# Performance work log

Hardware: AMD Instinct MI355X
Metric: run time of the kernel (lower is better)

## Reference

```python
import jax, jax.numpy as jnp
import numpy as np

# model dims
B, T, D, H, FF, L, V = 2, 1024, 1024, 16, 4096, 2, 32000
DH = D // H          # head dim 64
M = 32               # num attention blocks
BS = T // M          # block size 32
TOPK = 8             # quality-selected blocks per batch element
RATIO = 0.25         # low-pass ratio for spectral quality score
THETA = 10000.0      # rope base
EPS = 1e-6


def setup_inputs() -> dict:
    key = jax.random.key(0)
    ks = jax.random.split(key, 12)
    s = 0.02
    f32 = jnp.float32
    return {
        "input_ids": jax.random.randint(ks[0], (B, T), 0, V),
        "emb": jax.random.normal(ks[1], (V, D), f32) * s,
        "wq": jax.random.normal(ks[2], (L, D, D), f32) * s,
        "wk": jax.random.normal(ks[3], (L, D, D), f32) * s,
        "wv": jax.random.normal(ks[4], (L, D, D), f32) * s,
        "wo": jax.random.normal(ks[5], (L, D, D), f32) * s,
        "w1": jax.random.normal(ks[6], (L, D, FF), f32) * s,
        "w2": jax.random.normal(ks[7], (L, FF, D), f32) * s,
        "w3": jax.random.normal(ks[8], (L, D, FF), f32) * s,
        "attn_norm": jnp.ones((L, D), f32),
        "ffn_norm": jnp.ones((L, D), f32),
        "final_norm": jnp.ones((D,), f32),
        "lm_head": jax.random.normal(ks[9], (D, V), f32) * s,
    }


def _rms(x, w):
    return x * jax.lax.rsqrt(jnp.mean(x * x, axis=-1, keepdims=True) + EPS) * w


def _rope_tables():
    inv = 1.0 / (THETA ** (jnp.arange(0, DH, 2, dtype=jnp.float32) / DH))
    pos = jnp.arange(T, dtype=jnp.float32)
    freqs = pos[:, None] * inv[None, :]            # [T, DH/2]
    emb = jnp.concatenate([freqs, freqs], axis=-1)  # [T, DH]
    return jnp.cos(emb)[None, None], jnp.sin(emb)[None, None]  # [1,1,T,DH]


def _rotate_half(x):
    h = x.shape[-1] // 2
    return jnp.concatenate([-x[..., h:], x[..., :h]], axis=-1)


def _quality_score(h):
    # spectral quality rho(t): low-frequency energy ratio along the sequence axis
    Hf = jnp.fft.rfft(h, axis=1)                   # [B, T//2+1, D] complex
    nf = Hf.shape[1]
    keep = max(1, int(nf * RATIO))
    lp_mask = (jnp.arange(nf) < keep)[None, :, None]
    h_lp = jnp.fft.irfft(jnp.where(lp_mask, Hf, 0.0), n=T, axis=1)
    return jnp.sum(h_lp * h_lp, axis=-1) / (jnp.sum(h * h, axis=-1) + EPS)  # [B,T]


def _forward(input_ids, emb, wq, wk, wv, wo, w1, w2, w3,
             attn_norm, ffn_norm, final_norm, lm_head):
    x = emb[input_ids]                             # [B,T,D]

    # per-token quality (computed once, cached across layers) -> block quality
    rho = _quality_score(x)                        # [B,T]
    blk_quality = rho.reshape(B, M, BS).mean(axis=-1)  # [B,M]

    # quality routing: select top-k blocks per batch element
    _, sel_idx = jax.lax.top_k(blk_quality, TOPK)  # [B,TOPK]
    selected = jnp.zeros((B, M), dtype=bool).at[jnp.arange(B)[:, None], sel_idx].set(True)

    # block-sparse causal mask: causal AND (kv block selected OR same block as query)
    blk_id = jnp.arange(T) // BS                   # [T]
    causal = jnp.tril(jnp.ones((T, T), dtype=bool))
    same_block = blk_id[:, None] == blk_id[None, :]
    allowed_kv = selected[:, blk_id]               # [B,T]
    mask = causal[None] & (allowed_kv[:, None, :] | same_block[None])  # [B,T,T]
    bias = jnp.where(mask, 0.0, -1e9)[:, None]     # [B,1,T,T]

    cos, sin = _rope_tables()
    scale = 1.0 / np.sqrt(DH)

    for l in range(L):
        # attention
        h = _rms(x, attn_norm[l])
        q = (h @ wq[l]).reshape(B, T, H, DH).transpose(0, 2, 1, 3)
        k = (h @ wk[l]).reshape(B, T, H, DH).transpose(0, 2, 1, 3)
        v = (h @ wv[l]).reshape(B, T, H, DH).transpose(0, 2, 1, 3)
        q = q * cos + _rotate_half(q) * sin
        k = k * cos + _rotate_half(k) * sin
        scores = jnp.einsum('bhqd,bhkd->bhqk', q, k) * scale + bias
        attn = jax.nn.softmax(scores, axis=-1)
        o = jnp.einsum('bhqk,bhkd->bhqd', attn, v).transpose(0, 2, 1, 3).reshape(B, T, D)
        x = x + o @ wo[l]
        # swiglu feed-forward
        h = _rms(x, ffn_norm[l])
        x = x + (jax.nn.silu(h @ w1[l]) * (h @ w3[l])) @ w2[l]

    x = _rms(x, final_norm)
    return x @ lm_head                             # [B,T,V]


def reference(input_ids, emb, wq, wk, wv, wo, w1, w2, w3,
              attn_norm, ffn_norm, final_norm, lm_head):
    return _forward(input_ids, emb, wq, wk, wv, wo, w1, w2, w3,
                    attn_norm, ffn_norm, final_norm, lm_head)
```

## Files before the change

kernel.cpp:

```cpp
#include <hip/hip_runtime.h>
#include <hip/hip_bf16.h>

#define Bn 2
#define Tn 1024
#define Dn 1024
#define Hn 16
#define DHn 64
#define FFn 4096
#define Ln 2
#define Vn 32000
#define GM 2048

typedef unsigned short u16;
typedef __attribute__((ext_vector_type(4))) float f4;
typedef __attribute__((ext_vector_type(4))) unsigned short us4;
typedef __attribute__((ext_vector_type(8))) unsigned short us8;
typedef __attribute__((ext_vector_type(8))) short short8;
typedef __attribute__((ext_vector_type(4))) float f32x4;

__device__ __forceinline__ u16 f2b(float x) {
  union { __hip_bfloat16 h; u16 u; } v; v.h = __float2bfloat16(x); return v.u;
}
__device__ __forceinline__ float b2f(u16 u) {
  union { unsigned int i; float f; } v; v.i = ((unsigned int)u) << 16; return v.f;
}
__device__ __forceinline__ float wred64(float v) {
#pragma unroll
  for (int m = 32; m > 0; m >>= 1) v += __shfl_xor(v, m);
  return v;
}
__device__ __forceinline__ void gload_lds16(const void* g, void* l) {
  __builtin_amdgcn_global_load_lds(
      (const __attribute__((address_space(1))) unsigned int*)g,
      (__attribute__((address_space(3))) unsigned int*)l, 16, 0, 0);
}

__global__ void rope_tab_kernel(float* COS, float* SIN) {
  int t = blockIdx.x;
  int j = threadIdx.x;
  float inv = __expf(-(float)(j & 31) * (9.210340371976184f / 32.f));
  float th = (float)t * inv;
  COS[t * 64 + j] = cosf(th);
  SIN[t * 64 + j] = sinf(th);
}

__global__ __launch_bounds__(256) void embed_kernel(const int* ids, const float* emb, float* x) {
  int g = blockIdx.x;
  int id = ids[g];
  const f4* src = (const f4*)(emb + (size_t)id * Dn);
  f4* dst = (f4*)(x + (size_t)g * Dn);
  dst[threadIdx.x] = src[threadIdx.x];
}

__global__ __launch_bounds__(256) void qa_kernel(const float* x, float* Ac, float* Bc) {
  __shared__ float ct[1024], st[1024];
  int blk = blockIdx.x;
  int b = blk >> 7, f = blk & 127;
  for (int t = threadIdx.x; t < 1024; t += 256) {
    float u = (float)((f * t) & 1023) * (6.283185307179586f / 1024.f);
    ct[t] = cosf(u); st[t] = sinf(u);
  }
  __syncthreads();
  int d0 = threadIdx.x * 4;
  f4 a = {0.f,0.f,0.f,0.f}, bb = {0.f,0.f,0.f,0.f};
  const float* xb = x + (size_t)b * Tn * Dn + d0;
  for (int t = 0; t < 1024; ++t) {
    f4 xv = *(const f4*)(xb + (size_t)t * Dn);
    float c = ct[t], s = st[t];
    a += xv * c; bb += xv * s;
  }
  size_t o = ((size_t)b * 128 + f) * Dn + d0;
  *(f4*)(Ac + o) = a; *(f4*)(Bc + o) = bb;
}

__global__ __launch_bounds__(256) void qr_kernel(const float* Ac, const float* Bc,
                                                 const float* x, float* rho) {
  __shared__ float phc[128][4], phs[128][4];
  __shared__ float redN[4], redD[4];
  int blk = blockIdx.x;
  int b = blk >> 8, t0 = (blk & 255) * 4;
  int tid = threadIdx.x;
#pragma unroll
  for (int rep = 0; rep < 2; ++rep) {
    int e = rep * 256 + tid;
    int f = e >> 2, tt = e & 3;
    float u = (float)((f * (t0 + tt)) & 1023) * (6.283185307179586f / 1024.f);
    phc[f][tt] = cosf(u); phs[f][tt] = sinf(u);
  }
  int d0 = tid * 4;
  const float* Ab = Ac + (size_t)b * 128 * Dn + d0;
  const float* Bb = Bc + (size_t)b * 128 * Dn + d0;
  f4 a0 = *(const f4*)Ab;
  float sacc[4][4];
#pragma unroll
  for (int tt = 0; tt < 4; ++tt)
#pragma unroll
    for (int c = 0; c < 4; ++c) sacc[tt][c] = 0.5f * a0[c];
  __syncthreads();
  for (int f = 1; f < 128; ++f) {
    f4 a = *(const f4*)(Ab + (size_t)f * Dn);
    f4 bb = *(const f4*)(Bb + (size_t)f * Dn);
#pragma unroll
    for (int tt = 0; tt < 4; ++tt) {
      float c = phc[f][tt], s = phs[f][tt];
#pragma unroll
      for (int e = 0; e < 4; ++e) sacc[tt][e] += a[e] * c + bb[e] * s;
    }
  }
  int wave = tid >> 6, lane = tid & 63;
  for (int tt = 0; tt < 4; ++tt) {
    f4 xv = *(const f4*)(x + ((size_t)b * Tn + t0 + tt) * Dn + d0);
    float num = 0.f, den = 0.f;
#pragma unroll
    for (int e = 0; e < 4; ++e) {
      float hl = sacc[tt][e] * (2.f / 1024.f);
      num += hl * hl;
      den += xv[e] * xv[e];
    }
    float rn = wred64(num), rd = wred64(den);
    if (lane == 0) { redN[wave] = rn; redD[wave] = rd; }
    __syncthreads();
    if (tid == 0) {
      float n = redN[0] + redN[1] + redN[2] + redN[3];
      float dd = redD[0] + redD[1] + redD[2] + redD[3];
      rho[(size_t)b * Tn + t0 + tt] = n / (dd + 1e-6f);
    }
    __syncthreads();
  }
}

__global__ void topk_kernel(const float* rho, int* sel) {
  __shared__ float bq[32];
  __shared__ int chosen[32];
  int b = blockIdx.x;
  int m = threadIdx.x;
  float s = 0.f;
  for (int j = 0; j < 32; ++j) s += rho[(size_t)b * Tn + m * 32 + j];
  bq[m] = s * (1.f / 32.f); chosen[m] = 0;
  __syncthreads();
  if (m == 0) {
    for (int it = 0; it < 8; ++it) {
      float best = -3e38f; int bi = 0;
      for (int mm = 0; mm < 32; ++mm) if (bq[mm] > best) { best = bq[mm]; bi = mm; }
      chosen[bi] = 1; bq[bi] = -3e38f;
    }
  }
  __syncthreads();
  sel[b * 32 + m] = chosen[m];
}

__global__ __launch_bounds__(256) void transpose64(const float* __restrict__ src, u16* __restrict__ dst,
                                                   int K, int N, int rowmul, int rowadd) {
  __shared__ u16 tile[64][72];
  const int n0 = blockIdx.x * 64, k0 = blockIdx.y * 64;
  const int tid = threadIdx.x;
  const int r = tid >> 2;
  const int c0 = (tid & 3) * 16;
  const float* s = src + (size_t)(k0 + r) * N + n0 + c0;
#pragma unroll
  for (int q = 0; q < 4; ++q) {
    f4 v = *(const f4*)(s + q * 4);
#pragma unroll
    for (int e = 0; e < 4; ++e) tile[c0 + q * 4 + e][r] = f2b(v[e]);
  }
  __syncthreads();
  const int n = n0 + r;
  const size_t drow = (size_t)((n >> 4) * rowmul + rowadd + (n & 15));
  us8* d = (us8*)(dst + drow * K + k0 + c0);
  us8 o0, o1;
#pragma unroll
  for (int e = 0; e < 8; ++e) { o0[e] = tile[r][c0 + e]; o1[e] = tile[r][c0 + 8 + e]; }
  d[0] = o0; d[1] = o1;
}

__global__ __launch_bounds__(256) void rmsnorm_kernel(const float* x, const float* w, u16* out) {
  __shared__ float red[4];
  int g = blockIdx.x;
  int tid = threadIdx.x;
  f4 xv = ((const f4*)(x + (size_t)g * Dn))[tid];
  float ss = xv[0]*xv[0] + xv[1]*xv[1] + xv[2]*xv[2] + xv[3]*xv[3];
  ss = wred64(ss);
  if ((tid & 63) == 0) red[tid >> 6] = ss;
  __syncthreads();
  float tot = red[0] + red[1] + red[2] + red[3];
  float r = rsqrtf(tot * (1.f / 1024.f) + 1e-6f);
  f4 wv = ((const f4*)w)[tid];
  us4 o;
#pragma unroll
  for (int e = 0; e < 4; ++e) o[e] = f2b(xv[e] * r * wv[e]);
  *(us4*)(out + (size_t)g * Dn + tid * 4) = o;
}

template<int EPI>
__global__ __launch_bounds__(256) void gemm_bf16(
    const u16* __restrict__ A, const u16* __restrict__ Bt,
    float* C, const float* R, u16* U,
    float* QRo, float* KRo, float* VRo, const float* __restrict__ COS, const float* __restrict__ SIN,
    int Ni, int Ki, int cf) {
  __shared__ short8 As[1024];
  __shared__ short8 Bs[1024];
  const int tid = threadIdx.x;
  const int wave = tid >> 6, lane = tid & 63;
  const int wr = wave >> 1, wc = wave & 1;
  const int lrow = lane & 15, lkg = lane >> 4;
  const int lg = (blockIdx.x & 7) * ((int)gridDim.x >> 3) + ((int)blockIdx.x >> 3);
  int bx, by;
  if (cf) { const int nbx = Ni >> 7; bx = lg % nbx; by = lg / nbx; }
  else    { by = lg & 15; bx = lg >> 4; }
  const size_t arow0 = (size_t)by * 128;
  const size_t bcol0 = (size_t)bx * 128;
  const f32x4 zero4 = {0.f, 0.f, 0.f, 0.f};
  f32x4 acc[4][4];
#pragma unroll
  for (int i = 0; i < 4; ++i)
#pragma unroll
    for (int j = 0; j < 4; ++j) acc[i][j] = zero4;
  const int nK = Ki >> 6;
  for (int kb = 0; kb < nK; ++kb) {
    const size_t k0 = (size_t)kb << 6;
#pragma unroll
    for (int j = 0; j < 4; ++j) {
      const int p = j * 256 + tid;
      const int r = p >> 3, c = p & 7;
      const int cs = c ^ (r & 7);
      gload_lds16(A + (arow0 + r) * Ki + k0 + cs * 8, (char*)As + p * 16);
      gload_lds16(Bt + (bcol0 + r) * Ki + k0 + cs * 8, (char*)Bs + p * 16);
    }
    __syncthreads();
#pragma unroll
    for (int kk = 0; kk < 2; ++kk) {
      short8 af[4], bfr[4];
#pragma unroll
      for (int i = 0; i < 4; ++i) {
        const int ar = wr * 64 + i * 16 + lrow;
        const int akg = kk * 4 + lkg;
        af[i] = *(const short8*)((const char*)As + ar * 128 + ((akg ^ (ar & 7)) << 4));
        const int br = wc * 64 + i * 16 + lrow;
        bfr[i] = *(const short8*)((const char*)Bs + br * 128 + ((akg ^ (br & 7)) << 4));
      }
#pragma unroll
      for (int i = 0; i < 4; ++i)
#pragma unroll
        for (int j = 0; j < 4; ++j)
          acc[i][j] = __builtin_amdgcn_mfma_f32_16x16x32_bf16(af[i], bfr[j], acc[i][j], 0, 0, 0);
    }
    __syncthreads();
  }
  const int crow = (lane >> 4) * 4;
  const int ccol = lane & 15;
  if (EPI == 0) {
#pragma unroll
    for (int i = 0; i < 4; ++i)
#pragma unroll
      for (int j = 0; j < 4; ++j)
#pragma unroll
        for (int rg = 0; rg < 4; ++rg) {
          const size_t grow = arow0 + wr * 64 + i * 16 + crow + rg;
          const size_t gcol = bcol0 + wc * 64 + j * 16 + ccol;
          float v = acc[i][j][rg];
          if (R) v += R[grow * Ni + gcol];
          C[grow * Ni + gcol] = v;
        }
  } else if (EPI == 2) {
    const int sec = (int)(bcol0 >> 10);
    const int hh = (((int)bcol0 & 1023) >> 6) + wc;
    float* dstQK = (sec == 0) ? QRo : KRo;
#pragma unroll
    for (int i = 0; i < 4; ++i)
#pragma unroll
      for (int rg = 0; rg < 4; ++rg) {
        const int t = (int)arow0 + wr * 64 + i * 16 + crow + rg;
        const int bb = t >> 10, tt = t & 1023;
        const size_t obase = ((size_t)(bb * Hn + hh) * Tn + tt) * 64;
#pragma unroll
        for (int j = 0; j < 4; ++j) {
          const int jd = j * 16 + ccol;
          const float v = acc[i][j][rg];
          if (sec < 2) {
            const float p = acc[i][j ^ 2][rg];
            const float cs = COS[tt * 64 + jd], sn = SIN[tt * 64 + jd];
            dstQK[obase + jd] = v * cs + ((j < 2) ? -p : p) * sn;
          } else {
            VRo[obase + jd] = v;
          }
        }
      }
  } else if (EPI == 3) {
#pragma unroll
    for (int i = 0; i < 4; ++i)
#pragma unroll
      for (int rg = 0; rg < 4; ++rg) {
        const size_t grow = arow0 + wr * 64 + i * 16 + crow + rg;
#pragma unroll
        for (int jp = 0; jp < 2; ++jp) {
          const int j = jp * 2;
          const float a = acc[i][j][rg];
          const float g3 = acc[i][j + 1][rg];
          const float s = (a / (1.f + __expf(-a))) * g3;
          const int f = ((((int)bcol0 + wc * 64 + j * 16) >> 5) << 4) + ccol;
          U[grow * 4096 + f] = f2b(s);
        }
      }
  }
}

__global__ __launch_bounds__(256) void attn_kernel(
    const float* __restrict__ QR, const float* __restrict__ KR, const float* __restrict__ VR,
    const int* __restrict__ sel, u16* __restrict__ O) {
  __shared__ float Qs[32][64], Ks[32][64], Vs[32][64], S[32][32];
  const int blk = blockIdx.x;
  const int mq = blk & 31, h = (blk >> 5) & 15, b = blk >> 9;
  const int tid = threadIdx.x;
  const size_t bh = (size_t)(b * Hn + h) * Tn;
  {
    const f4* q4 = (const f4*)(QR + (bh + mq * 32) * 64);
    f4* s4 = (f4*)&Qs[0][0];
    s4[tid] = q4[tid]; s4[tid + 256] = q4[tid + 256];
  }
  const int row = tid >> 3, dg = tid & 7;
  const int dh0 = dg * 8;
  f4 acc0 = {0.f,0.f,0.f,0.f}, acc1 = {0.f,0.f,0.f,0.f};
  float m_i = -3e38f, l_i = 0.f;
  for (int mk = 0; mk <= mq; ++mk) {
    if (!(sel[b * 32 + mk] | (mk == mq))) continue;
    __syncthreads();
    {
      const f4* k4 = (const f4*)(KR + (bh + mk * 32) * 64);
      const f4* v4 = (const f4*)(VR + (bh + mk * 32) * 64);
      ((f4*)Ks)[tid] = k4[tid]; ((f4*)Ks)[tid + 256] = k4[tid + 256];
      ((f4*)Vs)[tid] = v4[tid]; ((f4*)Vs)[tid + 256] = v4[tid + 256];
    }
    __syncthreads();
#pragma unroll
    for (int c = 0; c < 4; ++c) {
      const int idx = tid * 4 + c;
      const int qi = idx >> 5, kj = idx & 31;
      const f4* qv = (const f4*)Qs[qi];
      const f4* kv = (const f4*)Ks[kj];
      f4 sv = {0.f,0.f,0.f,0.f};
#pragma unroll
      for (int d = 0; d < 16; ++d) sv += qv[d] * kv[d];
      float s = (sv[0] + sv[1] + sv[2] + sv[3]) * 0.125f;
      if (mk == mq && kj > qi) s = -3e38f;
      S[qi][kj] = s;
    }
    __syncthreads();
    float mx = m_i;
#pragma unroll
    for (int j2 = 0; j2 < 32; ++j2) mx = fmaxf(mx, S[row][j2]);
    const float resc = __expf(m_i - mx);
    float pv[4]; float psum = 0.f;
#pragma unroll
    for (int c = 0; c < 4; ++c) {
      pv[c] = __expf(S[row][dg * 4 + c] - mx);
      psum += pv[c];
    }
    __syncthreads();
#pragma unroll
    for (int c = 0; c < 4; ++c) S[row][dg * 4 + c] = pv[c];
    psum += __shfl_xor(psum, 1);
    psum += __shfl_xor(psum, 2);
    psum += __shfl_xor(psum, 4);
    l_i = l_i * resc + psum;
    m_i = mx;
    acc0 *= resc; acc1 *= resc;
    __syncthreads();
#pragma unroll
    for (int kj = 0; kj < 32; ++kj) {
      const float p = S[row][kj];
      const f4* vv = (const f4*)&Vs[kj][dh0];
      acc0 += vv[0] * p; acc1 += vv[1] * p;
    }
  }
  const float inv = 1.f / l_i;
  us8 o;
#pragma unroll
  for (int e = 0; e < 4; ++e) { o[e] = f2b(acc0[e] * inv); o[4 + e] = f2b(acc1[e] * inv); }
  const int t = mq * 32 + row;
  *(us8*)(O + (size_t)(b * Tn + t) * Dn + h * 64 + dh0) = o;
}

extern "C" void kernel_launch(void* const* d_in, const int* in_sizes, int n_in,
                              void* d_out, int out_size, void* d_ws, size_t ws_size,
                              hipStream_t stream) {
  const int*   ids   = (const int*)d_in[0];
  const float* emb   = (const float*)d_in[1];
  const float* wq    = (const float*)d_in[2];
  const float* wk    = (const float*)d_in[3];
  const float* wv    = (const float*)d_in[4];
  const float* wo    = (const float*)d_in[5];
  const float* w1    = (const float*)d_in[6];
  const float* w2    = (const float*)d_in[7];
  const float* w3    = (const float*)d_in[8];
  const float* anrm  = (const float*)d_in[9];
  const float* fnrm  = (const float*)d_in[10];
  const float* finrm = (const float*)d_in[11];
  const float* lmw   = (const float*)d_in[12];
  float* out = (float*)d_out;

  char* ws = (char*)d_ws;
  size_t off = 0;
  auto alloc = [&](size_t sz) { void* p = ws + off; off += (sz + 255) & ~(size_t)255; return p; };
  const size_t MB = 1024ull * 1024ull;

  float* X    = (float*)alloc((size_t)GM * Dn * 4);
  u16*   Hb   = (u16*)alloc((size_t)GM * Dn * 2);
  float* COS  = (float*)alloc((size_t)Tn * 64 * 4);
  float* SIN  = (float*)alloc((size_t)Tn * 64 * 4);
  int*   SEL  = (int*)alloc(256);
  u16*   QKVl = (u16*)alloc((size_t)3072 * 1024 * 2);
  u16*   WOl  = (u16*)alloc((size_t)1024 * 1024 * 2);
  u16*   W13l = (u16*)alloc((size_t)8192 * 1024 * 2);
  u16*   W2l  = (u16*)alloc((size_t)1024 * 4096 * 2);
  char*  SCR  = (char*)alloc(66 * MB);

  if (off > ws_size) return;

  float* Ac  = (float*)SCR;
  float* Bc  = (float*)(SCR + 1 * MB);
  float* RHO = (float*)(SCR + 2 * MB);
  float* QRb  = (float*)(SCR + 24 * MB);
  float* KRb  = (float*)(SCR + 32 * MB);
  float* VRb  = (float*)(SCR + 40 * MB);
  u16*   Ob   = (u16*)(SCR + 48 * MB);
  u16*   Ub   = (u16*)(SCR + 0 * MB);
  u16*   LMT  = (u16*)SCR;

  rope_tab_kernel<<<Tn, 64, 0, stream>>>(COS, SIN);
  embed_kernel<<<GM, 256, 0, stream>>>(ids, emb, X);
  qa_kernel<<<Bn * 128, 256, 0, stream>>>(X, Ac, Bc);
  qr_kernel<<<Bn * 256, 256, 0, stream>>>(Ac, Bc, X, RHO);
  topk_kernel<<<Bn, 32, 0, stream>>>(RHO, SEL);

  for (int l = 0; l < Ln; ++l) {
    const size_t dd = (size_t)1024 * 1024;
    const size_t df = (size_t)1024 * 4096;
    transpose64<<<dim3(16, 16), 256, 0, stream>>>(wq + l * dd, QKVl, 1024, 1024, 16, 0);
    transpose64<<<dim3(16, 16), 256, 0, stream>>>(wk + l * dd, QKVl + dd, 1024, 1024, 16, 0);
    transpose64<<<dim3(16, 16), 256, 0, stream>>>(wv + l * dd, QKVl + 2 * dd, 1024, 1024, 16, 0);
    transpose64<<<dim3(16, 16), 256, 0, stream>>>(wo + l * dd, WOl, 1024, 1024, 16, 0);
    transpose64<<<dim3(64, 16), 256, 0, stream>>>(w1 + l * df, W13l, 1024, 4096, 32, 0);
    transpose64<<<dim3(64, 16), 256, 0, stream>>>(w3 + l * df, W13l, 1024, 4096, 32, 16);
    transpose64<<<dim3(16, 64), 256, 0, stream>>>(w2 + l * df, W2l, 4096, 1024, 16, 0);

    rmsnorm_kernel<<<GM, 256, 0, stream>>>(X, anrm + l * Dn, Hb);
    gemm_bf16<2><<<384, 256, 0, stream>>>(Hb, QKVl, nullptr, nullptr, nullptr,
                                          QRb, KRb, VRb, COS, SIN, 3072, 1024, 0);
    attn_kernel<<<Bn * Hn * 32, 256, 0, stream>>>(QRb, KRb, VRb, SEL, Ob);
    gemm_bf16<0><<<128, 256, 0, stream>>>(Ob, WOl, X, X, nullptr,
                                          nullptr, nullptr, nullptr, nullptr, nullptr, 1024, 1024, 1);
    rmsnorm_kernel<<<GM, 256, 0, stream>>>(X, fnrm + l * Dn, Hb);
    gemm_bf16<3><<<1024, 256, 0, stream>>>(Hb, W13l, nullptr, nullptr, Ub,
                                           nullptr, nullptr, nullptr, nullptr, nullptr, 8192, 1024, 0);
    gemm_bf16<0><<<128, 256, 0, stream>>>(Ub, W2l, X, X, nullptr,
                                          nullptr, nullptr, nullptr, nullptr, nullptr, 1024, 4096, 1);
  }

  transpose64<<<dim3(500, 16), 256, 0, stream>>>(lmw, LMT, 1024, Vn, 16, 0);
  rmsnorm_kernel<<<GM, 256, 0, stream>>>(X, finrm, Hb);
  gemm_bf16<0><<<4000, 256, 0, stream>>>(Hb, LMT, out, nullptr, nullptr,
                                         nullptr, nullptr, nullptr, nullptr, nullptr, Vn, 1024, 0);
}
```

Baseline: 1.582 ms.

## Split spectral projection over time chunks, double-buffer GEMM LDS, nontemporal stores

The spectral-projection kernel now splits the sequence into 8 time chunks, giving 2048 blocks instead of 256. A new reduction kernel sums the chunk partials, which exposes more parallelism at the cost of extra partial-buffer traffic and one more launch. The bf16 GEMM double-buffers its LDS tiles so the next K-tile loads are issued before the current tile's MFMAs run. GEMM outputs with no residual are now written with nontemporal stores. The extra LDS doubles shared memory per block, which may lower occupancy.

```diff
diff --git a/kernel.cpp b/kernel.cpp
--- a/kernel.cpp
+++ b/kernel.cpp
@@ -52,25 +52,44 @@
   dst[threadIdx.x] = src[threadIdx.x];
 }
 
-__global__ __launch_bounds__(256) void qa_kernel(const float* x, float* Ac, float* Bc) {
-  __shared__ float ct[1024], st[1024];
+__global__ __launch_bounds__(256) void qa_kernel(const float* __restrict__ x,
+                                                 float* __restrict__ PA, float* __restrict__ PB) {
+  __shared__ float ct[128], st[128];
   int blk = blockIdx.x;
-  int b = blk >> 7, f = blk & 127;
-  for (int t = threadIdx.x; t < 1024; t += 256) {
+  int tc = blk & 7, f = (blk >> 3) & 127, b = blk >> 10;
+  int t0 = tc * 128;
+  if (threadIdx.x < 128) {
+    int t = t0 + threadIdx.x;
     float u = (float)((f * t) & 1023) * (6.283185307179586f / 1024.f);
-    ct[t] = cosf(u); st[t] = sinf(u);
+    ct[threadIdx.x] = cosf(u); st[threadIdx.x] = sinf(u);
   }
   __syncthreads();
   int d0 = threadIdx.x * 4;
   f4 a = {0.f,0.f,0.f,0.f}, bb = {0.f,0.f,0.f,0.f};
-  const float* xb = x + (size_t)b * Tn * Dn + d0;
-  for (int t = 0; t < 1024; ++t) {
+  const float* xb = x + ((size_t)b * Tn + t0) * Dn + d0;
+  for (int t = 0; t < 128; ++t) {
     f4 xv = *(const f4*)(xb + (size_t)t * Dn);
     float c = ct[t], s = st[t];
     a += xv * c; bb += xv * s;
   }
-  size_t o = ((size_t)b * 128 + f) * Dn + d0;
-  *(f4*)(Ac + o) = a; *(f4*)(Bc + o) = bb;
+  size_t o = (((size_t)b * 128 + f) * 8 + tc) * Dn + d0;
+  *(f4*)(PA + o) = a; *(f4*)(PB + o) = bb;
+}
+
+__global__ __launch_bounds__(256) void qa_red_kernel(const float* __restrict__ PA, const float* __restrict__ PB,
+                                                     float* __restrict__ Ac, float* __restrict__ Bc) {
+  int blk = blockIdx.x;
+  int d0 = threadIdx.x * 4;
+  const float* pa = PA + ((size_t)blk * 8) * Dn + d0;
+  const float* pb = PB + ((size_t)blk * 8) * Dn + d0;
+  f4 a = {0.f,0.f,0.f,0.f}, bb = {0.f,0.f,0.f,0.f};
+#pragma unroll
+  for (int tc = 0; tc < 8; ++tc) {
+    a += *(const f4*)(pa + (size_t)tc * Dn);
+    bb += *(const f4*)(pb + (size_t)tc * Dn);
+  }
+  *(f4*)(Ac + (size_t)blk * Dn + d0) = a;
+  *(f4*)(Bc + (size_t)blk * Dn + d0) = bb;
 }
 
 __global__ __launch_bounds__(256) void qr_kernel(const float* Ac, const float* Bc,
@@ -197,8 +216,8 @@
     float* C, const float* R, u16* U,
     float* QRo, float* KRo, float* VRo, const float* __restrict__ COS, const float* __restrict__ SIN,
     int Ni, int Ki, int cf) {
-  __shared__ short8 As[1024];
-  __shared__ short8 Bs[1024];
+  __shared__ short8 As[2][1024];
+  __shared__ short8 Bs[2][1024];
   const int tid = threadIdx.x;
   const int wave = tid >> 6, lane = tid & 63;
   const int wr = wave >> 1, wc = wave & 1;
@@ -209,6 +228,8 @@
   else    { by = lg & 15; bx = lg >> 4; }
   const size_t arow0 = (size_t)by * 128;
   const size_t bcol0 = (size_t)bx * 128;
+  const int p0 = tid * 4;
+  (void)p0;
   const f32x4 zero4 = {0.f, 0.f, 0.f, 0.f};
   f32x4 acc[4][4];
 #pragma unroll
@@ -216,17 +237,24 @@
 #pragma unroll
     for (int j = 0; j < 4; ++j) acc[i][j] = zero4;
   const int nK = Ki >> 6;
-  for (int kb = 0; kb < nK; ++kb) {
+
+  auto STAGE = [&](int buf, int kb) {
     const size_t k0 = (size_t)kb << 6;
 #pragma unroll
     for (int j = 0; j < 4; ++j) {
       const int p = j * 256 + tid;
       const int r = p >> 3, c = p & 7;
       const int cs = c ^ (r & 7);
-      gload_lds16(A + (arow0 + r) * Ki + k0 + cs * 8, (char*)As + p * 16);
-      gload_lds16(Bt + (bcol0 + r) * Ki + k0 + cs * 8, (char*)Bs + p * 16);
-    }
-    __syncthreads();
+      gload_lds16(A + (arow0 + r) * Ki + k0 + cs * 8, (char*)&As[buf][0] + p * 16);
+      gload_lds16(Bt + (bcol0 + r) * Ki + k0 + cs * 8, (char*)&Bs[buf][0] + p * 16);
+    }
+  };
+
+  STAGE(0, 0);
+  __syncthreads();
+  int cur = 0;
+  for (int kb = 0; kb < nK; ++kb) {
+    if (kb + 1 < nK) STAGE(cur ^ 1, kb + 1);
 #pragma unroll
     for (int kk = 0; kk < 2; ++kk) {
       short8 af[4], bfr[4];
@@ -234,9 +262,9 @@
       for (int i = 0; i < 4; ++i) {
         const int ar = wr * 64 + i * 16 + lrow;
         const int akg = kk * 4 + lkg;
-        af[i] = *(const short8*)((const char*)As + ar * 128 + ((akg ^ (ar & 7)) << 4));
+        af[i] = *(const short8*)((const char*)&As[cur][0] + ar * 128 + ((akg ^ (ar & 7)) << 4));
         const int br = wc * 64 + i * 16 + lrow;
-        bfr[i] = *(const short8*)((const char*)Bs + br * 128 + ((akg ^ (br & 7)) << 4));
+        bfr[i] = *(const short8*)((const char*)&Bs[cur][0] + br * 128 + ((akg ^ (br & 7)) << 4));
       }
 #pragma unroll
       for (int i = 0; i < 4; ++i)
@@ -245,7 +273,9 @@
           acc[i][j] = __builtin_amdgcn_mfma_f32_16x16x32_bf16(af[i], bfr[j], acc[i][j], 0, 0, 0);
     }
     __syncthreads();
-  }
+    cur ^= 1;
+  }
+
   const int crow = (lane >> 4) * 4;
   const int ccol = lane & 15;
   if (EPI == 0) {
@@ -258,8 +288,12 @@
           const size_t grow = arow0 + wr * 64 + i * 16 + crow + rg;
           const size_t gcol = bcol0 + wc * 64 + j * 16 + ccol;
           float v = acc[i][j][rg];
-          if (R) v += R[grow * Ni + gcol];
-          C[grow * Ni + gcol] = v;
+          if (R) {
+            v += R[grow * Ni + gcol];
+            C[grow * Ni + gcol] = v;
+          } else {
+            __builtin_nontemporal_store(v, &C[grow * Ni + gcol]);
+          }
         }
   } else if (EPI == 2) {
     const int sec = (int)(bcol0 >> 10);
@@ -419,6 +453,8 @@
   float* Ac  = (float*)SCR;
   float* Bc  = (float*)(SCR + 1 * MB);
   float* RHO = (float*)(SCR + 2 * MB);
+  float* PA  = (float*)(SCR + 4 * MB);
+  float* PB  = (float*)(SCR + 12 * MB);
   float* QRb  = (float*)(SCR + 24 * MB);
   float* KRb  = (float*)(SCR + 32 * MB);
   float* VRb  = (float*)(SCR + 40 * MB);
@@ -428,7 +464,8 @@
 
   rope_tab_kernel<<<Tn, 64, 0, stream>>>(COS, SIN);
   embed_kernel<<<GM, 256, 0, stream>>>(ids, emb, X);
-  qa_kernel<<<Bn * 128, 256, 0, stream>>>(X, Ac, Bc);
+  qa_kernel<<<2048, 256, 0, stream>>>(X, PA, PB);
+  qa_red_kernel<<<256, 256, 0, stream>>>(PA, PB, Ac, Bc);
   qr_kernel<<<Bn * 256, 256, 0, stream>>>(Ac, Bc, X, RHO);
   topk_kernel<<<Bn, 32, 0, stream>>>(RHO, SEL);
 
```

After: 1.499 ms. -5.3%, faster.
